# Performance work log

Measured on AMD Instinct MI355X. Metric: run time of the kernel, lower is better.

## Reference

```python
import jax, jax.numpy as jnp
import numpy as np

B, S, F, D, H, L, K = 64, 512, 8, 512, 8, 2, 512
FF = 4 * D
DH = D // H


def _ln(x):
    m = jnp.mean(x, axis=-1, keepdims=True)
    v = jnp.var(x, axis=-1, keepdims=True)
    return (x - m) * jax.lax.rsqrt(v + 1e-5)


def _encoder_layer(x, Wqkv, Wo, W1, b1, W2, b2):
    # pre-LN multi-head self-attention
    h = _ln(x)
    qkv = h @ Wqkv                                   # [B,S,3D]
    q, k, v = jnp.split(qkv, 3, axis=-1)
    q = q.reshape(B, S, H, DH)
    k = k.reshape(B, S, H, DH)
    v = v.reshape(B, S, H, DH)
    scores = jnp.einsum('bqhd,bkhd->bhqk', q, k) / jnp.sqrt(jnp.float32(DH))
    attn = jax.nn.softmax(scores, axis=-1)
    o = jnp.einsum('bhqk,bkhd->bqhd', attn, v).reshape(B, S, D) @ Wo
    x = x + o
    # pre-LN feed-forward
    h = _ln(x)
    x = x + (jax.nn.relu(h @ W1 + b1) @ W2 + b2)
    return x


def setup_inputs() -> dict:
    key = jax.random.key(0)
    ks = jax.random.split(key, 12)
    sc = 0.02
    inp = {
        'x': jax.random.normal(ks[0], (B, S, F), dtype=jnp.float32),
        'enc_W': jax.random.normal(ks[1], (F, D), dtype=jnp.float32) * sc,
        'enc_b': jnp.zeros((D,), dtype=jnp.float32),
        'Wqkv': jax.random.normal(ks[2], (L, D, 3 * D), dtype=jnp.float32) * sc,
        'Wo': jax.random.normal(ks[3], (L, D, D), dtype=jnp.float32) * sc,
        'W1': jax.random.normal(ks[4], (L, D, FF), dtype=jnp.float32) * sc,
        'b1': jnp.zeros((L, FF), dtype=jnp.float32),
        'W2': jax.random.normal(ks[5], (L, FF, D), dtype=jnp.float32) * sc,
        'b2': jnp.zeros((L, D), dtype=jnp.float32),
        'centers': jax.random.normal(ks[6], (K, D), dtype=jnp.float32),
    }
    return inp


def reference(x, enc_W, enc_b, Wqkv, Wo, W1, b1, W2, b2, centers):
    # enc_embedding
    h = x @ enc_W + enc_b                            # [B,S,D]
    # seq_model: stack of standard transformer encoder layers
    for i in range(L):
        h = _encoder_layer(h, Wqkv[i], Wo[i], W1[i], b1[i], W2[i], b2[i])
    output_seq = h                                   # [B,S,D]
    # torch.cdist(output_seq, centers, p=2) via matmul expansion
    on2 = jnp.sum(output_seq * output_seq, axis=-1, keepdims=True)   # [B,S,1]
    cn2 = jnp.sum(centers * centers, axis=-1)                        # [K]
    dist2 = on2 + cn2[None, None, :] - 2.0 * jnp.einsum('bsd,kd->bsk', output_seq, centers)
    cluster_ids = jnp.argmin(dist2, axis=-1)                         # [B,S]
    assigned_centroids = centers[cluster_ids]                        # [B,S,D] gather
    diff = output_seq - assigned_centroids
    # torch.norm(diff, dim=1)**2 then mean == mean over (B,D) of sum over S of diff^2
    loss = jnp.mean(jnp.sum(diff * diff, axis=1))
    return loss, output_seq
```

## Files before the change

### kernel.cpp

```cpp
#include <hip/hip_runtime.h>
#include <cstdint>
#include <cstddef>

typedef __attribute__((ext_vector_type(4))) float f32x4;
typedef __attribute__((ext_vector_type(8))) short s16x8;
typedef __attribute__((ext_vector_type(4))) short s16x4;

__device__ __forceinline__ short f2bf(float f){
  unsigned u; __builtin_memcpy(&u, &f, 4);
  u += 0x7fffu + ((u >> 16) & 1u);
  return (short)(u >> 16);
}

__device__ __forceinline__ void gll16(const void* g, void* l) {
  auto* lp = (__attribute__((address_space(3))) unsigned*)(uintptr_t)(l);
  const auto* gp = (const __attribute__((address_space(1))) unsigned*)(uintptr_t)(g);
  __builtin_amdgcn_global_load_lds(gp, lp, 16, 0, 0);
}

__device__ __forceinline__ void ds_tr8(unsigned a, s16x4* r) {
  asm volatile(
    "ds_read_b64_tr_b16 %0, %8\n\t"
    "ds_read_b64_tr_b16 %1, %8 offset:512\n\t"
    "ds_read_b64_tr_b16 %2, %8 offset:2048\n\t"
    "ds_read_b64_tr_b16 %3, %8 offset:2560\n\t"
    "ds_read_b64_tr_b16 %4, %8 offset:4096\n\t"
    "ds_read_b64_tr_b16 %5, %8 offset:4608\n\t"
    "ds_read_b64_tr_b16 %6, %8 offset:6144\n\t"
    "ds_read_b64_tr_b16 %7, %8 offset:6656\n\t"
    "s_waitcnt lgkmcnt(0)"
    : "=&v"(r[0]), "=&v"(r[1]), "=&v"(r[2]), "=&v"(r[3]),
      "=&v"(r[4]), "=&v"(r[5]), "=&v"(r[6]), "=&v"(r[7])
    : "v"(a)
    : "memory");
}

__global__ __launch_bounds__(256) void encode_kernel(
    const float* __restrict__ x, const float* __restrict__ W,
    const float* __restrict__ b, float* __restrict__ out)
{
  const int t = blockIdx.x;
  float xv[8];
#pragma unroll
  for (int f = 0; f < 8; ++f) xv[f] = x[(size_t)t*8 + f];
  for (int d = threadIdx.x; d < 512; d += 256) {
    float acc = b[d];
#pragma unroll
    for (int f = 0; f < 8; ++f) acc += xv[f] * W[f*512 + d];
    out[(size_t)t*512 + d] = acc;
  }
}

__global__ __launch_bounds__(256) void ln_kernel(
    const float* __restrict__ x, short* __restrict__ out)
{
  const int w = threadIdx.x >> 6, lane = threadIdx.x & 63;
  const int t = blockIdx.x * 4 + w;
  const float* row = x + (size_t)t * 512;
  float4 v0 = *(const float4*)&row[lane*8];
  float4 v1 = *(const float4*)&row[lane*8 + 4];
  float vals[8] = {v0.x,v0.y,v0.z,v0.w,v1.x,v1.y,v1.z,v1.w};
  float s = 0.f, sq = 0.f;
#pragma unroll
  for (int i = 0; i < 8; ++i) { s += vals[i]; sq += vals[i]*vals[i]; }
#pragma unroll
  for (int m = 1; m < 64; m <<= 1) { s += __shfl_xor(s, m); sq += __shfl_xor(sq, m); }
  float mean = s * (1.f/512.f);
  float var  = sq * (1.f/512.f) - mean*mean;
  float rstd = rsqrtf(var + 1e-5f);
  s16x8 o;
#pragma unroll
  for (int i = 0; i < 8; ++i) o[i] = f2bf((vals[i]-mean)*rstd);
  *(s16x8*)&out[(size_t)t*512 + lane*8] = o;
}

__global__ __launch_bounds__(256) void transpose_bf16_kernel(
    const float* __restrict__ in, short* __restrict__ out, int K, int N, int kshift)
{
  const int o = blockIdx.x * 256 + threadIdx.x;
  const int k = o & (K - 1), n = o >> kshift;
  out[o] = f2bf(in[(size_t)k * N + n]);
}

__global__ __launch_bounds__(256) void convert_bf16_kernel(
    const float* __restrict__ in, short* __restrict__ out)
{
  const int i = blockIdx.x * 256 + threadIdx.x;
  out[i] = f2bf(in[i]);
}

template<bool BIAS, bool RELU, bool RESID, bool OUT32>
__global__ __launch_bounds__(512, 1) void gemm_kernel(
    const short* __restrict__ A, const short* __restrict__ Bt,
    void* Cout, const float* __restrict__ bias,
    const float* resid, int M, int N, int K)
{
  __shared__ short As[4][256 * 32];
  __shared__ short Bs[4][256 * 32];
  const int tid = threadIdx.x;
  const int lane = tid & 63, w = tid >> 6;
  const int wr = w >> 2, wc = w & 3;
  const int q = lane & 15, g = lane >> 4;

  const int nx = gridDim.x;
  const int d = blockIdx.y * nx + blockIdx.x;
  const int per = (nx * gridDim.y) >> 3;
  const int lid = (d & 7) * per + (d >> 3);
  const int bx = lid % nx, by = lid / nx;
  const int m0 = by * 256, n0 = bx * 256;

  const int srow = lane >> 2;
  const int scol = (((lane & 3) ^ ((lane >> 4) & 3)) * 8);
  const short* aS0 = A  + (size_t)(m0 + w*32 + srow) * K + scol;
  const short* aS1 = aS0 + (size_t)16 * K;
  const short* bS0 = Bt + (size_t)(n0 + w*32 + srow) * K + scol;
  const short* bS1 = bS0 + (size_t)16 * K;
  const int d0 = (w*2) * 512, d1 = (w*2 + 1) * 512;

  const int gs = (g ^ (q >> 2)) * 8;

  f32x4 acc[8][4] = {};
  const int nt = K >> 5;

  auto STAGE = [&](int tt) {
    const int k0 = tt << 5;
    const int nb = tt & 3;
    gll16(aS0 + k0, &As[nb][d0]);
    gll16(aS1 + k0, &As[nb][d1]);
    gll16(bS0 + k0, &Bs[nb][d0]);
    gll16(bS1 + k0, &Bs[nb][d1]);
  };
  auto COMPUTE = [&](int t) {
    const int bufc = t & 3;
    if (t + 3 < nt) STAGE(t + 3);
    s16x8 aF[8], bF[4];
#pragma unroll
    for (int i = 0; i < 8; ++i) aF[i] = *(const s16x8*)&As[bufc][(wr*128 + i*16 + q)*32 + gs];
#pragma unroll
    for (int i = 0; i < 4; ++i) bF[i] = *(const s16x8*)&Bs[bufc][(wc*64 + i*16 + q)*32 + gs];
#pragma unroll
    for (int mi = 0; mi < 8; ++mi)
#pragma unroll
      for (int ni = 0; ni < 4; ++ni)
        acc[mi][ni] = __builtin_amdgcn_mfma_f32_16x16x32_bf16(aF[mi], bF[ni], acc[mi][ni], 0, 0, 0);
  };

  STAGE(0); STAGE(1); STAGE(2);

  for (int t = 0; t < nt - 2; ++t) {
    asm volatile("s_waitcnt vmcnt(8)" ::: "memory");
    __builtin_amdgcn_s_barrier();
    __builtin_amdgcn_sched_barrier(0);
    COMPUTE(t);
    __builtin_amdgcn_sched_barrier(0);
  }
  asm volatile("s_waitcnt vmcnt(4)" ::: "memory");
  __builtin_amdgcn_s_barrier();
  __builtin_amdgcn_sched_barrier(0);
  COMPUTE(nt - 2);
  asm volatile("s_waitcnt vmcnt(0)" ::: "memory");
  __builtin_amdgcn_s_barrier();
  __builtin_amdgcn_sched_barrier(0);
  COMPUTE(nt - 1);

#pragma unroll
  for (int mi = 0; mi < 8; ++mi) {
#pragma unroll
    for (int r = 0; r < 4; ++r) {
      const int gr = m0 + wr*128 + mi*16 + g*4 + r;
#pragma unroll
      for (int ni = 0; ni < 4; ++ni) {
        const int gc = n0 + wc*64 + ni*16 + q;
        float v = acc[mi][ni][r];
        if (BIAS) v += bias[gc];
        if (RELU) v = fmaxf(v, 0.f);
        if (RESID) v += resid[(size_t)gr * N + gc];
        if (OUT32) ((float*)Cout)[(size_t)gr * N + gc] = v;
        else       ((short*)Cout)[(size_t)gr * N + gc] = f2bf(v);
      }
    }
  }
}

__global__ __launch_bounds__(256) void attn_kernel(
    const short* __restrict__ qkv, short* __restrict__ attn_out)
{
  __shared__ short Ks[2][64 * 64];
  __shared__ short Vs[2][64 * 64];
  const int tid = threadIdx.x;
  const int w = tid >> 6, lane = tid & 63;
  const int q16 = lane & 15, g = lane >> 4;
  const int dd = blockIdx.x;
  const int lid = (dd & 7) * (int)(gridDim.x >> 3) + (dd >> 3);
  const int qt4 = lid & 7, h = (lid >> 3) & 7, b = lid >> 6;
  const size_t base = (size_t)b * 512 * 1536;
  const int qrow = qt4*64 + w*16 + q16;

  s16x8 bQ0, bQ1;
  {
    const size_t p = base + (size_t)qrow * 1536 + h*64 + g*8;
    bQ0 = *(const s16x8*)&qkv[p];
    bQ1 = *(const s16x8*)&qkv[p + 32];
  }

  const int c0 = w*2, c1 = w*2 + 1;
  const short* kS0 = qkv + base + (size_t)(c0*8 + (lane>>3))*1536 + 512 + h*64 + ((lane&7)^(lane>>3))*8;
  const short* kS1 = qkv + base + (size_t)(c1*8 + (lane>>3))*1536 + 512 + h*64 + ((lane&7)^(lane>>3))*8;
  const short* vS0 = qkv + base + (size_t)((c0&1)*32 + (lane>>1))*1536 + 1024 + h*64 + (c0>>1)*16 + (lane&1)*8;
  const short* vS1 = qkv + base + (size_t)((c1&1)*32 + (lane>>1))*1536 + 1024 + h*64 + (c1>>1)*16 + (lane&1)*8;

  const unsigned vs_lane = (unsigned)(size_t)(&Vs[0][0]) + (unsigned)((q16 + g*64)*2);
  const int sw = q16 & 7;

  float mrun = -1e30f, ssum = 0.f;
  f32x4 O[4] = {};

  gll16(kS0, &Ks[0][c0*512]);
  gll16(kS1, &Ks[0][c1*512]);
  gll16(vS0, &Vs[0][c0*512]);
  gll16(vS1, &Vs[0][c1*512]);
  __syncthreads();

  int cur = 0;
  for (int j0 = 0; j0 < 512; j0 += 64) {
    s16x8 ka0[4], ka1[4];
#pragma unroll
    for (int grp = 0; grp < 4; ++grp) {
      const int rb = (grp*16 + q16) * 64;
      ka0[grp] = *(const s16x8*)&Ks[cur][rb + ((g    ) ^ sw)*8];
      ka1[grp] = *(const s16x8*)&Ks[cur][rb + ((g + 4) ^ sw)*8];
    }
    if (j0 + 64 < 512) {
      const size_t joff = (size_t)(j0 + 64) * 1536;
      const int nxt = cur ^ 1;
      gll16(kS0 + joff, &Ks[nxt][c0*512]);
      gll16(kS1 + joff, &Ks[nxt][c1*512]);
      gll16(vS0 + joff, &Vs[nxt][c0*512]);
      gll16(vS1 + joff, &Vs[nxt][c1*512]);
    }
    __builtin_amdgcn_sched_barrier(0);

    f32x4 c[4];
#pragma unroll
    for (int grp = 0; grp < 4; ++grp) {
      f32x4 z = {};
      c[grp] = __builtin_amdgcn_mfma_f32_16x16x32_bf16(ka0[grp], bQ0, z, 0, 0, 0);
      c[grp] = __builtin_amdgcn_mfma_f32_16x16x32_bf16(ka1[grp], bQ1, c[grp], 0, 0, 0);
    }

    float sc[16];
#pragma unroll
    for (int grp = 0; grp < 4; ++grp)
#pragma unroll
      for (int r = 0; r < 4; ++r) sc[grp*4 + r] = c[grp][r] * 0.125f;
    float bm = sc[0];
#pragma unroll
    for (int i = 1; i < 16; ++i) bm = fmaxf(bm, sc[i]);
    bm = fmaxf(bm, __shfl_xor(bm, 16));
    bm = fmaxf(bm, __shfl_xor(bm, 32));
    const float mn = fmaxf(mrun, bm);
    const float alpha = __expf(mrun - mn);
    float p[16]; float bs = 0.f;
#pragma unroll
    for (int i = 0; i < 16; ++i) { p[i] = __expf(sc[i] - mn); bs += p[i]; }
    bs += __shfl_xor(bs, 16);
    bs += __shfl_xor(bs, 32);
    ssum = ssum * alpha + bs;
    mrun = mn;
#pragma unroll
    for (int db = 0; db < 4; ++db) O[db] *= alpha;

#pragma unroll
    for (int kk = 0; kk < 2; ++kk) {
      s16x8 pf;
#pragma unroll
      for (int e = 0; e < 8; ++e) pf[e] = f2bf(p[(kk*2 + (e >> 2))*4 + (e & 3)]);
      s16x4 r[8];
      ds_tr8(vs_lane + (unsigned)(cur << 13) + (unsigned)(kk*1024), r);
      __builtin_amdgcn_sched_barrier(0);
#pragma unroll
      for (int db = 0; db < 4; ++db) {
        s16x8 vf = __builtin_shufflevector(r[2*db], r[2*db + 1], 0, 1, 2, 3, 4, 5, 6, 7);
        O[db] = __builtin_amdgcn_mfma_f32_16x16x32_bf16(vf, pf, O[db], 0, 0, 0);
      }
    }
    __syncthreads();
    cur ^= 1;
  }

  const float inv = 1.f / ssum;
  const size_t tok = (size_t)b*512 + qrow;
#pragma unroll
  for (int db = 0; db < 4; ++db) {
    s16x4 ov;
#pragma unroll
    for (int r = 0; r < 4; ++r) ov[r] = f2bf(O[db][r] * inv);
    *(s16x4*)&attn_out[tok*512 + h*64 + db*16 + g*4] = ov;
  }
}

__global__ __launch_bounds__(256) void finalize_seq_kernel(
    const float* __restrict__ resid, float* __restrict__ outseq, short* __restrict__ obf)
{
  const size_t i = (size_t)blockIdx.x * 256 + threadIdx.x;
  const float v = resid[i];
  outseq[i] = v;
  obf[i] = f2bf(v);
}

__global__ __launch_bounds__(256) void cn2_kernel(
    const float* __restrict__ centers, float* __restrict__ cn2)
{
  const int c = blockIdx.x;
  __shared__ float red[256];
  float s = 0.f;
  for (int d = threadIdx.x; d < 512; d += 256) { float v = centers[(size_t)c*512 + d]; s += v*v; }
  red[threadIdx.x] = s; __syncthreads();
  for (int off = 128; off > 0; off >>= 1) {
    if (threadIdx.x < off) red[threadIdx.x] += red[threadIdx.x + off];
    __syncthreads();
  }
  if (threadIdx.x == 0) cn2[c] = red[0];
}

__global__ __launch_bounds__(256) void argmin_kernel(
    const float* __restrict__ gdist, const float* __restrict__ cn2,
    const float* __restrict__ resid, const float* __restrict__ centers,
    float* __restrict__ partial)
{
  const int w = threadIdx.x >> 6, lane = threadIdx.x & 63;
  const int t = blockIdx.x * 4 + w;
  float best = 1e30f; int bi = 0;
#pragma unroll
  for (int j = 0; j < 8; ++j) {
    const int k = j*64 + lane;
    const float v = cn2[k] - 2.f * gdist[(size_t)t*512 + k];
    if (v < best || (v == best && k < bi)) { best = v; bi = k; }
  }
#pragma unroll
  for (int mm = 1; mm < 64; mm <<= 1) {
    const float ov = __shfl_xor(best, mm); const int oi = __shfl_xor(bi, mm);
    if (ov < best || (ov == best && oi < bi)) { best = ov; bi = oi; }
  }
  float s = 0.f;
#pragma unroll
  for (int j = 0; j < 2; ++j) {
    float4 o = *(const float4*)&resid[(size_t)t*512 + lane*8 + j*4];
    float4 c = *(const float4*)&centers[(size_t)bi*512 + lane*8 + j*4];
    const float dx = o.x-c.x, dy = o.y-c.y, dz = o.z-c.z, dw = o.w-c.w;
    s += dx*dx + dy*dy + dz*dz + dw*dw;
  }
#pragma unroll
  for (int mm = 1; mm < 64; mm <<= 1) s += __shfl_xor(s, mm);
  __shared__ float red[4];
  if (lane == 0) red[w] = s;
  __syncthreads();
  if (threadIdx.x == 0) partial[blockIdx.x] = red[0] + red[1] + red[2] + red[3];
}

__global__ __launch_bounds__(256) void loss_kernel(
    const float* __restrict__ partial, int n, float* __restrict__ out)
{
  float s = 0.f;
  for (int i = threadIdx.x; i < n; i += 256) s += partial[i];
  __shared__ float red[256];
  red[threadIdx.x] = s; __syncthreads();
  for (int off = 128; off > 0; off >>= 1) {
    if (threadIdx.x < off) red[threadIdx.x] += red[threadIdx.x + off];
    __syncthreads();
  }
  if (threadIdx.x == 0) out[0] = red[0] * (1.f / 32768.f);
}

extern "C" void kernel_launch(void* const* d_in, const int* in_sizes, int n_in,
                              void* d_out, int out_size, void* d_ws, size_t ws_size,
                              hipStream_t stream) {
  const float* x     = (const float*)d_in[0];
  const float* enc_W = (const float*)d_in[1];
  const float* enc_b = (const float*)d_in[2];
  const float* Wqkv  = (const float*)d_in[3];
  const float* Wo    = (const float*)d_in[4];
  const float* W1    = (const float*)d_in[5];
  const float* b1    = (const float*)d_in[6];
  const float* W2    = (const float*)d_in[7];
  const float* b2    = (const float*)d_in[8];
  const float* cen   = (const float*)d_in[9];
  float* out = (float*)d_out;

  const int NT = 32768;
  char* ws = (char*)d_ws;
  float* resid   = (float*)(ws);
  short* h_ln    = (short*)(ws + 67108864);
  char*  pool    = ws + 100663296;
  short* qkv     = (short*)pool;
  short* attn_o  = (short*)(pool + 100663296);
  short* hidden  = (short*)pool;
  float* gdist   = (float*)pool;
  short* wbase   = (short*)(ws + 234881024);
  short* wqT     = wbase;
  short* woT     = wbase + 1572864;
  short* w1T     = wbase + 2097152;
  short* w2T     = wbase + 4194304;
  short* cenb    = wbase + 6291456;
  float* cn2     = (float*)(ws + 247988224);
  float* partial = (float*)(ws + 247990272);

  for (int l = 0; l < 2; ++l) {
    transpose_bf16_kernel<<<3072, 256, 0, stream>>>(Wqkv + (size_t)l*512*1536, wqT + (size_t)l*786432, 512, 1536, 9);
    transpose_bf16_kernel<<<1024, 256, 0, stream>>>(Wo   + (size_t)l*512*512,  woT + (size_t)l*262144, 512, 512, 9);
    transpose_bf16_kernel<<<4096, 256, 0, stream>>>(W1   + (size_t)l*512*2048, w1T + (size_t)l*1048576, 512, 2048, 9);
    transpose_bf16_kernel<<<4096, 256, 0, stream>>>(W2   + (size_t)l*2048*512, w2T + (size_t)l*1048576, 2048, 512, 11);
  }
  convert_bf16_kernel<<<1024, 256, 0, stream>>>(cen, cenb);
  cn2_kernel<<<512, 256, 0, stream>>>(cen, cn2);

  encode_kernel<<<NT, 256, 0, stream>>>(x, enc_W, enc_b, resid);

  for (int l = 0; l < 2; ++l) {
    ln_kernel<<<NT/4, 256, 0, stream>>>(resid, h_ln);
    gemm_kernel<false,false,false,false><<<dim3(6, 128), 512, 0, stream>>>(
        h_ln, wqT + (size_t)l*786432, qkv, nullptr, nullptr, NT, 1536, 512);
    attn_kernel<<<4096, 256, 0, stream>>>(qkv, attn_o);
    gemm_kernel<false,false,true,true><<<dim3(2, 128), 512, 0, stream>>>(
        attn_o, woT + (size_t)l*262144, resid, nullptr, resid, NT, 512, 512);
    ln_kernel<<<NT/4, 256, 0, stream>>>(resid, h_ln);
    gemm_kernel<true,true,false,false><<<dim3(8, 128), 512, 0, stream>>>(
        h_ln, w1T + (size_t)l*1048576, hidden, b1 + (size_t)l*2048, nullptr, NT, 2048, 512);
    gemm_kernel<true,false,true,true><<<dim3(2, 128), 512, 0, stream>>>(
        hidden, w2T + (size_t)l*1048576, resid, b2 + (size_t)l*512, resid, NT, 512, 2048);
  }

  finalize_seq_kernel<<<65536, 256, 0, stream>>>(resid, out + 1, h_ln);
  gemm_kernel<false,false,false,true><<<dim3(2, 128), 512, 0, stream>>>(
      h_ln, cenb, gdist, nullptr, nullptr, NT, 512, 512);
  argmin_kernel<<<NT/4, 256, 0, stream>>>(gdist, cn2, resid, cen, partial);
  loss_kernel<<<1, 256, 0, stream>>>(partial, NT/4, out);
}
```

Baseline: 944.6 us.

## Load GEMM B fragments directly to registers and raise MFMA wave priority

The GEMM stops staging the B tile through shared memory. Each wave now loads its B fragments straight from global memory into registers, double-buffered one step ahead, while A keeps a shallower LDS pipeline that runs two stages ahead instead of three. This halves LDS usage and removes the LDS reads for B, at the cost of redundant global B loads across the two waves that share a column and more register pressure. The MFMA sections in both the GEMM and the attention kernel are also wrapped with s_setprio so those waves get scheduling priority.

```diff
diff --git a/kernel.cpp b/kernel.cpp
--- a/kernel.cpp
+++ b/kernel.cpp
@@ -96,7 +96,6 @@
     const float* resid, int M, int N, int K)
 {
   __shared__ short As[4][256 * 32];
-  __shared__ short Bs[4][256 * 32];
   const int tid = threadIdx.x;
   const int lane = tid & 63, w = tid >> 6;
   const int wr = w >> 2, wc = w & 3;
@@ -111,57 +110,57 @@
 
   const int srow = lane >> 2;
   const int scol = (((lane & 3) ^ ((lane >> 4) & 3)) * 8);
-  const short* aS0 = A  + (size_t)(m0 + w*32 + srow) * K + scol;
+  const short* aS0 = A + (size_t)(m0 + w*32 + srow) * K + scol;
   const short* aS1 = aS0 + (size_t)16 * K;
-  const short* bS0 = Bt + (size_t)(n0 + w*32 + srow) * K + scol;
-  const short* bS1 = bS0 + (size_t)16 * K;
   const int d0 = (w*2) * 512, d1 = (w*2 + 1) * 512;
 
   const int gs = (g ^ (q >> 2)) * 8;
+
+  const short* bp = Bt + (size_t)(n0 + wc*64 + q) * K + g*8;
 
   f32x4 acc[8][4] = {};
   const int nt = K >> 5;
 
-  auto STAGE = [&](int tt) {
-    const int k0 = tt << 5;
-    const int nb = tt & 3;
+  auto STAGE_A = [&](int tt) {
+    const int k0 = tt << 5, nb = tt & 3;
     gll16(aS0 + k0, &As[nb][d0]);
     gll16(aS1 + k0, &As[nb][d1]);
-    gll16(bS0 + k0, &Bs[nb][d0]);
-    gll16(bS1 + k0, &Bs[nb][d1]);
   };
-  auto COMPUTE = [&](int t) {
-    const int bufc = t & 3;
-    if (t + 3 < nt) STAGE(t + 3);
-    s16x8 aF[8], bF[4];
-#pragma unroll
-    for (int i = 0; i < 8; ++i) aF[i] = *(const s16x8*)&As[bufc][(wr*128 + i*16 + q)*32 + gs];
-#pragma unroll
-    for (int i = 0; i < 4; ++i) bF[i] = *(const s16x8*)&Bs[bufc][(wc*64 + i*16 + q)*32 + gs];
-#pragma unroll
-    for (int mi = 0; mi < 8; ++mi)
-#pragma unroll
-      for (int ni = 0; ni < 4; ++ni)
-        acc[mi][ni] = __builtin_amdgcn_mfma_f32_16x16x32_bf16(aF[mi], bF[ni], acc[mi][ni], 0, 0, 0);
+  s16x8 bcur[4], bnxt[4];
+  auto LOADB = [&](int tt, s16x8* bf) {
+    const int k0 = tt << 5;
+#pragma unroll
+    for (int i = 0; i < 4; ++i)
+      bf[i] = *(const s16x8*)&bp[(size_t)(i*16) * K + k0];
   };
 
-  STAGE(0); STAGE(1); STAGE(2);
-
-  for (int t = 0; t < nt - 2; ++t) {
-    asm volatile("s_waitcnt vmcnt(8)" ::: "memory");
+  STAGE_A(0);
+  LOADB(0, bcur);
+  STAGE_A(1);
+
+  for (int t = 0; t < nt; ++t) {
+    if (t < nt - 1) asm volatile("s_waitcnt vmcnt(6)" ::: "memory");
+    else            asm volatile("s_waitcnt vmcnt(4)" ::: "memory");
     __builtin_amdgcn_s_barrier();
     __builtin_amdgcn_sched_barrier(0);
-    COMPUTE(t);
+    if (t + 1 < nt) LOADB(t + 1, bnxt);
     __builtin_amdgcn_sched_barrier(0);
-  }
-  asm volatile("s_waitcnt vmcnt(4)" ::: "memory");
-  __builtin_amdgcn_s_barrier();
-  __builtin_amdgcn_sched_barrier(0);
-  COMPUTE(nt - 2);
-  asm volatile("s_waitcnt vmcnt(0)" ::: "memory");
-  __builtin_amdgcn_s_barrier();
-  __builtin_amdgcn_sched_barrier(0);
-  COMPUTE(nt - 1);
+    if (t + 2 < nt) STAGE_A(t + 2);
+    __builtin_amdgcn_sched_barrier(0);
+    const short* Ab = &As[t & 3][0];
+    s16x8 aF[8];
+#pragma unroll
+    for (int i = 0; i < 8; ++i) aF[i] = *(const s16x8*)&Ab[(wr*128 + i*16 + q)*32 + gs];
+    __builtin_amdgcn_s_setprio(1);
+#pragma unroll
+    for (int mi = 0; mi < 8; ++mi)
+#pragma unroll
+      for (int ni = 0; ni < 4; ++ni)
+        acc[mi][ni] = __builtin_amdgcn_mfma_f32_16x16x32_bf16(aF[mi], bcur[ni], acc[mi][ni], 0, 0, 0);
+    __builtin_amdgcn_s_setprio(0);
+#pragma unroll
+    for (int i = 0; i < 4; ++i) bcur[i] = bnxt[i];
+  }
 
 #pragma unroll
   for (int mi = 0; mi < 8; ++mi) {
@@ -241,12 +240,14 @@
     __builtin_amdgcn_sched_barrier(0);
 
     f32x4 c[4];
+    __builtin_amdgcn_s_setprio(1);
 #pragma unroll
     for (int grp = 0; grp < 4; ++grp) {
       f32x4 z = {};
       c[grp] = __builtin_amdgcn_mfma_f32_16x16x32_bf16(ka0[grp], bQ0, z, 0, 0, 0);
       c[grp] = __builtin_amdgcn_mfma_f32_16x16x32_bf16(ka1[grp], bQ1, c[grp], 0, 0, 0);
     }
+    __builtin_amdgcn_s_setprio(0);
 
     float sc[16];
 #pragma unroll
@@ -278,11 +279,13 @@
       s16x4 r[8];
       ds_tr8(vs_lane + (unsigned)(cur << 13) + (unsigned)(kk*1024), r);
       __builtin_amdgcn_sched_barrier(0);
+      __builtin_amdgcn_s_setprio(1);
 #pragma unroll
       for (int db = 0; db < 4; ++db) {
         s16x8 vf = __builtin_shufflevector(r[2*db], r[2*db + 1], 0, 1, 2, 3, 4, 5, 6, 7);
         O[db] = __builtin_amdgcn_mfma_f32_16x16x32_bf16(vf, pf, O[db], 0, 0, 0);
       }
+      __builtin_amdgcn_s_setprio(0);
     }
     __syncthreads();
     cur ^= 1;
```

New measurement: 1.197 ms. 1.27x slower.
